# Kernel optimization log

Hardware: AMD Instinct MI355X
Metric: run time of the kernel (lower is better)

Reference implementation:

```python
import jax, jax.numpy as jnp
import numpy as np

GRID_SIZE = 5
SPLINE_ORDER = 3
NB = GRID_SIZE + SPLINE_ORDER          # 8 basis functions
NG = GRID_SIZE + 2 * SPLINE_ORDER + 1  # 12 extended grid points
EPS = 1e-12


def make_grid(in_features):
    h = 2.0 / GRID_SIZE  # grid range [-1, 1]
    pts = (np.arange(-SPLINE_ORDER, GRID_SIZE + SPLINE_ORDER + 1) * h - 1.0).astype(np.float32)
    return jnp.asarray(np.tile(pts[None, :], (in_features, 1)))  # (in, NG)


def bspline_basis(x, grid):
    # x: (B, in), grid: (in, NG) -> (B, in, GRID_SIZE+SPLINE_ORDER)
    xe = x[..., None]
    bases = ((xe >= grid[:, :-1]) & (xe < grid[:, 1:])).astype(x.dtype)
    for k in range(1, SPLINE_ORDER + 1):
        left = (xe - grid[:, :-(k + 1)]) / (grid[:, k:-1] - grid[:, :-(k + 1)]) * bases[..., :-1]
        right = (grid[:, k + 1:] - xe) / (grid[:, k + 1:] - grid[:, 1:-k]) * bases[..., 1:]
        bases = left + right
    return bases


def kan_linear(x, grid, base_w, spline_w):
    # efficient-KAN layer: SiLU base branch + B-spline branch
    base = jax.nn.silu(x) @ base_w.T                      # (B, out)
    basis = bspline_basis(x, grid)                        # (B, in, NB)
    spline = jnp.einsum('big,oig->bo', basis, spline_w)   # (B, out)
    return base + spline


def l2norm(x):
    return x / jnp.maximum(jnp.linalg.norm(x, axis=1, keepdims=True), EPS)


def setup_inputs() -> dict:
    key = jax.random.key(0)
    ks = jax.random.split(key, 12)
    N = 2048
    x = jax.random.normal(ks[0], (N, 1, 529, 16), dtype=jnp.float32)
    xvaw = jax.random.normal(ks[1], (N, 16), dtype=jnp.float32)
    # KAN([529, 40, 60])
    grid1 = make_grid(529)
    base_w1 = jax.random.normal(ks[2], (40, 529), dtype=jnp.float32) * (1.0 / np.sqrt(529))
    spline_w1 = jax.random.normal(ks[3], (40, 529, NB), dtype=jnp.float32) * 0.1
    grid2 = make_grid(40)
    base_w2 = jax.random.normal(ks[4], (60, 40), dtype=jnp.float32) * (1.0 / np.sqrt(40))
    spline_w2 = jax.random.normal(ks[5], (60, 40, NB), dtype=jnp.float32) * 0.1
    # head: Linear(960,512) -> L2Norm -> spline_activation(512) -> Linear(512,16) -> L2Norm
    lin1_w = jax.random.normal(ks[6], (512, 960), dtype=jnp.float32) * (1.0 / np.sqrt(960))
    lin1_b = jnp.zeros((512,), dtype=jnp.float32)
    act_grid = make_grid(512)
    act_base = jnp.ones((512,), dtype=jnp.float32)
    act_coeff = jax.random.normal(ks[7], (512, NB), dtype=jnp.float32) * 0.1
    lin2_w = jax.random.normal(ks[8], (16, 512), dtype=jnp.float32) * (1.0 / np.sqrt(512))
    lin2_b = jnp.zeros((16,), dtype=jnp.float32)
    return {"x": x, "xvaw": xvaw, "grid1": grid1, "base_w1": base_w1, "spline_w1": spline_w1,
            "grid2": grid2, "base_w2": base_w2, "spline_w2": spline_w2,
            "lin1_w": lin1_w, "lin1_b": lin1_b, "act_grid": act_grid, "act_base": act_base,
            "act_coeff": act_coeff, "lin2_w": lin2_w, "lin2_b": lin2_b}


def reference(x, xvaw, grid1, base_w1, spline_w1, grid2, base_w2, spline_w2,
              lin1_w, lin1_b, act_grid, act_base, act_coeff, lin2_w, lin2_b):
    N = x.shape[0]
    W = x.shape[3]  # 16
    xa = jnp.transpose(x[:, 0], (2, 0, 1)).reshape(W * N, 529)  # batched over all W slices
    h = kan_linear(xa, grid1, base_w1, spline_w1)               # (W*N, 40)
    h = kan_linear(h, grid2, base_w2, spline_w2)                # (W*N, 60)
    h = jnp.transpose(h.reshape(W, N, 60), (1, 2, 0)).reshape(N, 60 * W)  # (N, 960)
    h = h @ lin1_w.T + lin1_b
    h = l2norm(h)
    # per-dim spline activation (KAN-style single activation)
    basis = bspline_basis(h, act_grid)                          # (N, 512, NB)
    h = act_base * jax.nn.silu(h) + jnp.einsum('bdg,dg->bd', basis, act_coeff)
    h = h @ lin2_w.T + lin2_b
    return l2norm(h)
```

## Files before the change

kernel.cpp:

```cpp
#include <hip/hip_runtime.h>


typedef short bf16x8 __attribute__((ext_vector_type(8)));
typedef float f32x16 __attribute__((ext_vector_type(16)));

__device__ __forceinline__ float siluf(float x) { return x / (1.f + __expf(-x)); }

__device__ __forceinline__ unsigned short f2bf_rne(float v) {
    union { float f; unsigned u; } a; a.f = v;
    return (unsigned short)((a.u + 0x7fffu + ((a.u >> 16) & 1u)) >> 16);
}
__device__ __forceinline__ float bf2f(unsigned short h) {
    union { unsigned u; float f; } a; a.u = ((unsigned)h) << 16;
    return a.f;
}

__device__ __forceinline__ void bspline8(float x, float fm[8]) {
    float tpos = (x + 2.2f) * 2.5f;
    float fc = floorf(tpos);
    int c = (int)fc;
    float u = tpos - fc;
    bool valid = (c >= 0) && (c <= 10);
    float om = 1.f - u;
    float u2 = u * u, u3 = u2 * u;
    float W0 = om * om * om * (1.f / 6.f);
    float W1 = (3.f * u3 - 6.f * u2 + 4.f) * (1.f / 6.f);
    float W2 = (-3.f * u3 + 3.f * u2 + 3.f * u + 1.f) * (1.f / 6.f);
    float W3 = u3 * (1.f / 6.f);
#pragma unroll
    for (int m = 0; m < 8; ++m) {
        int d = c - m;
        float v = (d == 3) ? W0 : 0.f;
        v = (d == 2) ? W1 : v;
        v = (d == 1) ? W2 : v;
        v = (d == 0) ? W3 : v;
        fm[m] = valid ? v : 0.f;
    }
}

__global__ __launch_bounds__(256) void k_prep(
    const float* __restrict__ base_w1, const float* __restrict__ spline_w1,
    const float* __restrict__ base_w2, const float* __restrict__ spline_w2,
    const float* __restrict__ lin1_w,
    unsigned short* __restrict__ bhi, unsigned short* __restrict__ blo,
    unsigned short* __restrict__ whi, unsigned short* __restrict__ wlo,
    float* __restrict__ w2t) {
    int gid = blockIdx.x * 256 + threadIdx.x;
    int stride = gridDim.x * 256;
    for (int idx = gid; idx < 529 * 2 * 512; idx += stride) {
        int j = idx & 7;
        int l = (idx >> 3) & 63;
        int nti = idx >> 9;
        int nt = nti & 1;
        int i = nti >> 1;
        int q = ((l >> 5) << 3) + j;
        int o = nt * 32 + (l & 31);
        float val = 0.f;
        if (o < 40 && q <= 8)
            val = (q == 0) ? base_w1[o * 529 + i]
                           : spline_w1[(o * 529 + i) * 8 + (q - 1)];
        unsigned short h = f2bf_rne(val);
        bhi[idx] = h;
        blo[idx] = f2bf_rne(val - bf2f(h));
    }
    for (int idx = gid; idx < 60 * 16 * 512; idx += stride) {
        int j = idx & 7;
        int l = (idx >> 3) & 63;
        int ctdq = idx >> 9;
        int ct = ctdq & 15;
        int dq = ctdq >> 4;
        int k = dq * 16 + ((l >> 5) << 3) + j;
        int u = ct * 32 + (l & 31);
        float val = lin1_w[(size_t)u * 960 + k];
        unsigned short h = f2bf_rne(val);
        whi[idx] = h;
        wlo[idx] = f2bf_rne(val - bf2f(h));
    }
    for (int idx = gid; idx < 40 * 540; idx += stride) {
        int i = idx / 540;
        int rem = idx - i * 540;
        int q = rem / 60;
        int o = rem - q * 60;
        w2t[idx] = (q == 0) ? base_w2[o * 40 + i]
                            : spline_w2[(o * 40 + i) * 8 + (q - 1)];
    }
}

__global__ __launch_bounds__(256) void k_l1(
    const float* __restrict__ x, const unsigned short* __restrict__ bhi,
    const unsigned short* __restrict__ blo, _Float16* __restrict__ h1p) {
    int t = threadIdx.x;
    int l = t & 63;
    int wv = t >> 6;
    int rb = blockIdx.x & 255;
    int split = blockIdx.x >> 8;
    int gr0 = rb * 128 + wv * 32;
    int col = l & 31;
    int g2 = l >> 5;
    int gr = gr0 + col;
    const float* xrow = x + (size_t)(gr >> 4) * 8464 + (gr & 15);

    f32x16 acc0, acc1;
#pragma unroll
    for (int r = 0; r < 16; ++r) { acc0[r] = 0.f; acc1[r] = 0.f; }

    int i_lo = split * 89;
    int i_hi = i_lo + 89 < 529 ? i_lo + 89 : 529;

    float xv_nxt = xrow[(size_t)i_lo * 16];
#pragma unroll 1
    for (int i = i_lo; i < i_hi; ++i) {
        float xv = xv_nxt;
        int inx = i + 1;
        xv_nxt = (inx < i_hi) ? xrow[(size_t)inx * 16] : 0.f;

        float s0 = siluf(xv);
        float fm[8];
        bspline8(xv, fm);

        float av[8];
        av[0] = g2 ? fm[7] : s0;
#pragma unroll
        for (int j = 1; j < 8; ++j) av[j] = g2 ? 0.f : fm[j - 1];

        bf16x8 ahi, alo;
#pragma unroll
        for (int j = 0; j < 8; ++j) {
            union { float f; unsigned u; } a; a.f = av[j];
            unsigned short h = (unsigned short)(a.u >> 16);
            ahi[j] = (short)h;
            union { float f; unsigned u; } r; r.f = av[j] - bf2f(h);
            alo[j] = (short)(r.u >> 16);
        }

        const bf16x8* bh = (const bf16x8*)(bhi + ((size_t)i * 2) * 512 + (size_t)l * 8);
        const bf16x8* bl = (const bf16x8*)(blo + ((size_t)i * 2) * 512 + (size_t)l * 8);
        bf16x8 bh0 = bh[0], bh1 = bh[64];
        bf16x8 bl0 = bl[0], bl1 = bl[64];

        acc0 = __builtin_amdgcn_mfma_f32_32x32x16_bf16(ahi, bh0, acc0, 0, 0, 0);
        acc1 = __builtin_amdgcn_mfma_f32_32x32x16_bf16(ahi, bh1, acc1, 0, 0, 0);
        acc0 = __builtin_amdgcn_mfma_f32_32x32x16_bf16(ahi, bl0, acc0, 0, 0, 0);
        acc1 = __builtin_amdgcn_mfma_f32_32x32x16_bf16(ahi, bl1, acc1, 0, 0, 0);
        acc0 = __builtin_amdgcn_mfma_f32_32x32x16_bf16(alo, bh0, acc0, 0, 0, 0);
        acc1 = __builtin_amdgcn_mfma_f32_32x32x16_bf16(alo, bh1, acc1, 0, 0, 0);
    }

    _Float16* hp = h1p + (size_t)split * 1310720;
#pragma unroll
    for (int reg = 0; reg < 16; ++reg) {
        int rl = (reg & 3) + 8 * (reg >> 2) + 4 * g2;
        size_t g = (size_t)(gr0 + rl);
        hp[g * 40 + col] = (_Float16)acc0[reg];
        if (col < 8) hp[g * 40 + 32 + col] = (_Float16)acc1[reg];
    }
}

__global__ __launch_bounds__(256) void k_l2(
    const _Float16* __restrict__ h1p, const float* __restrict__ w2t,
    float* __restrict__ h2d) {
    __shared__ float lds[256 * 41];
    int t = threadIdx.x;
    int rc = blockIdx.x >> 2;
    int oq = blockIdx.x & 3;
    size_t base = (size_t)rc * 10240;

#pragma unroll 1
    for (int e = t; e < 10240; e += 256) {
        int r = e / 40;
        int i = e - r * 40;
        float v = (float)h1p[base + e];
        v += (float)h1p[1310720 + base + e];
        v += (float)h1p[2621440 + base + e];
        v += (float)h1p[3932160 + base + e];
        v += (float)h1p[5242880 + base + e];
        v += (float)h1p[6553600 + base + e];
        lds[r * 41 + i] = v;
    }
    __syncthreads();

    float acc[15];
#pragma unroll
    for (int oo = 0; oo < 15; ++oo) acc[oo] = 0.f;

#pragma unroll 1
    for (int i = 0; i < 40; ++i) {
        float hv = lds[t * 41 + i];
        float f[9];
        f[0] = siluf(hv);
        bspline8(hv, f + 1);
        const float* wp = w2t + i * 540 + oq * 15;
#pragma unroll
        for (int q = 0; q < 9; ++q) {
            float fv = f[q];
#pragma unroll
            for (int oo = 0; oo < 15; ++oo)
                acc[oo] = fmaf(fv, wp[q * 60 + oo], acc[oo]);
        }
    }
    int gr = rc * 256 + t;
    int n = gr >> 4, w = gr & 15;
    float* op = h2d + (size_t)n * 960 + w;
#pragma unroll
    for (int oo = 0; oo < 15; ++oo)
        op[(size_t)(oq * 15 + oo) * 16] = acc[oo];
}

__global__ __launch_bounds__(256) void k3(
    const float* __restrict__ h2d, const unsigned short* __restrict__ whi,
    const unsigned short* __restrict__ wlo, const float* __restrict__ lin1_b,
    float* __restrict__ h3) {
    int t = threadIdx.x;
    int l = t & 63;
    int wv = t >> 6;
    int rt = blockIdx.x >> 2;
    int ct = (blockIdx.x & 3) * 4 + wv;
    int col = l & 31;
    int g2 = l >> 5;
    int row = rt * 32 + col;
    const float* hrow = h2d + (size_t)row * 960 + g2 * 8;

    f32x16 acc;
#pragma unroll
    for (int r = 0; r < 16; ++r) acc[r] = 0.f;

#pragma unroll 1
    for (int dq = 0; dq < 60; ++dq) {
        float4 a0 = *(const float4*)(hrow + dq * 16);
        float4 a1 = *(const float4*)(hrow + dq * 16 + 4);
        float av[8] = {a0.x, a0.y, a0.z, a0.w, a1.x, a1.y, a1.z, a1.w};

        bf16x8 ahi, alo;
#pragma unroll
        for (int j = 0; j < 8; ++j) {
            union { float f; unsigned u; } a; a.f = av[j];
            unsigned short h = (unsigned short)(a.u >> 16);
            ahi[j] = (short)h;
            union { float f; unsigned u; } r; r.f = av[j] - bf2f(h);
            alo[j] = (short)(r.u >> 16);
        }

        size_t boff = ((size_t)(dq * 16 + ct) * 64 + l) * 8;
        bf16x8 bhv = *(const bf16x8*)(whi + boff);
        bf16x8 blv = *(const bf16x8*)(wlo + boff);

        acc = __builtin_amdgcn_mfma_f32_32x32x16_bf16(ahi, bhv, acc, 0, 0, 0);
        acc = __builtin_amdgcn_mfma_f32_32x32x16_bf16(ahi, blv, acc, 0, 0, 0);
        acc = __builtin_amdgcn_mfma_f32_32x32x16_bf16(alo, bhv, acc, 0, 0, 0);
    }

    int u = ct * 32 + col;
    float bu = lin1_b[u];
#pragma unroll
    for (int reg = 0; reg < 16; ++reg) {
        int rl = (reg & 3) + 8 * (reg >> 2) + 4 * g2;
        h3[(size_t)(rt * 32 + rl) * 512 + u] = acc[reg] + bu;
    }
}

__global__ __launch_bounds__(512) void k4(
    const float* __restrict__ h3, const float* __restrict__ act_base,
    const float* __restrict__ act_coeff, const float* __restrict__ lin2_w,
    const float* __restrict__ lin2_b, float* __restrict__ out) {
    int t = threadIdx.x;
    int wv = t >> 6, lane = t & 63;
    int n = blockIdx.x * 8 + wv;
    const float* hr = h3 + (size_t)n * 512;

    float xv[8];
#pragma unroll
    for (int k = 0; k < 8; ++k) xv[k] = hr[lane + 64 * k];
    float ss = 0.f;
#pragma unroll
    for (int k = 0; k < 8; ++k) ss = fmaf(xv[k], xv[k], ss);
#pragma unroll
    for (int d = 1; d < 64; d <<= 1) ss += __shfl_xor(ss, d, 64);
    float scale = 1.f / fmaxf(sqrtf(ss), 1e-12f);

    float act[8];
#pragma unroll
    for (int k = 0; k < 8; ++k) {
        int u = lane + 64 * k;
        float hn = xv[k] * scale;
        float s = siluf(hn);
        float fm[8];
        bspline8(hn, fm);
        float4 c0 = *(const float4*)(act_coeff + (size_t)u * 8);
        float4 c1 = *(const float4*)(act_coeff + (size_t)u * 8 + 4);
        float a = act_base[u] * s;
        a = fmaf(fm[0], c0.x, a);
        a = fmaf(fm[1], c0.y, a);
        a = fmaf(fm[2], c0.z, a);
        a = fmaf(fm[3], c0.w, a);
        a = fmaf(fm[4], c1.x, a);
        a = fmaf(fm[5], c1.y, a);
        a = fmaf(fm[6], c1.z, a);
        a = fmaf(fm[7], c1.w, a);
        act[k] = a;
    }

    float y = 0.f;
#pragma unroll
    for (int v = 0; v < 16; ++v) {
        float pv = 0.f;
#pragma unroll
        for (int k = 0; k < 8; ++k)
            pv = fmaf(act[k], lin2_w[v * 512 + lane + 64 * k], pv);
#pragma unroll
        for (int d = 1; d < 64; d <<= 1) pv += __shfl_xor(pv, d, 64);
        if (lane == v) y = pv + lin2_b[v];
    }
    float qq = y * y;
#pragma unroll
    for (int d = 1; d < 16; d <<= 1) qq += __shfl_xor(qq, d, 64);
    float sc2 = 1.f / fmaxf(sqrtf(qq), 1e-12f);
    if (lane < 16)
        out[(size_t)n * 16 + lane] = y * sc2;
}

extern "C" void kernel_launch(void* const* d_in, const int* in_sizes, int n_in,
                              void* d_out, int out_size, void* d_ws,
                              size_t ws_size, hipStream_t stream) {
    auto find = [&](int sz, int occur) -> const float* {
        int seen = 0;
        for (int i = 0; i < n_in; ++i) {
            if (in_sizes[i] == sz) {
                if (seen == occur) return (const float*)d_in[i];
                ++seen;
            }
        }
        return nullptr;
    };
    const float* x         = find(17334272, 0);
    const float* base_w1   = find(21160, 0);
    const float* spline_w1 = find(169280, 0);
    const float* base_w2   = find(2400, 0);
    const float* spline_w2 = find(19200, 0);
    const float* lin1_w    = find(491520, 0);
    const float* lin1_b    = find(512, 0);
    const float* act_base  = find(512, 1);
    const float* act_coeff = find(4096, 0);
    const float* lin2_w    = find(8192, 0);
    const float* lin2_b    = find(16, 0);
    if (!x || !base_w1 || !spline_w1 || !base_w2 || !spline_w2 || !lin1_w ||
        !lin1_b || !act_base || !act_coeff || !lin2_w || !lin2_b) {
        x         = (const float*)d_in[0];
        base_w1   = (const float*)d_in[3];
        spline_w1 = (const float*)d_in[4];
        base_w2   = (const float*)d_in[6];
        spline_w2 = (const float*)d_in[7];
        lin1_w    = (const float*)d_in[8];
        lin1_b    = (const float*)d_in[9];
        act_base  = (const float*)d_in[11];
        act_coeff = (const float*)d_in[12];
        lin2_w    = (const float*)d_in[13];
        lin2_b    = (const float*)d_in[14];
    }

    char* ws = (char*)d_ws;
    float* w2t = (float*)ws;
    unsigned short* whi = (unsigned short*)(ws + 86400);
    unsigned short* wlo = (unsigned short*)(ws + 1069440);
    float* h2d = (float*)(ws + 2052480);
    unsigned short* bhi = (unsigned short*)(ws + 2052480);
    unsigned short* blo = bhi + 541696;
    _Float16* h1p = (_Float16*)(ws + 9916800);
    float* h3 = (float*)(ws + 25645440);

    k_prep<<<1024, 256, 0, stream>>>(base_w1, spline_w1, base_w2, spline_w2,
                                     lin1_w, bhi, blo, whi, wlo, w2t);
    k_l1<<<1536, 256, 0, stream>>>(x, bhi, blo, h1p);
    k_l2<<<512, 256, 0, stream>>>(h1p, w2t, h2d);
    k3<<<256, 256, 0, stream>>>(h2d, whi, wlo, lin1_b, h3);
    k4<<<256, 512, 0, stream>>>(h3, act_base, act_coeff, lin2_w, lin2_b,
                                (float*)d_out);
}
```

Before: 379.9 us.

## Pack layer-1 K dimension densely: separate base and spline GEMMs over packed inputs

Layer 1 used to spend one 16-wide MFMA K step per input feature with half the slots padded. It now runs a base GEMM over 16 inputs per step (34 steps) and a spline GEMM that packs two inputs' 8 basis values per step (265 steps). The weight prep builds matching repacked bf16 hi/lo tables. This roughly halves the MFMA count and weight loads. k_l2 now reduces the split partials with vectorized per-row f16x8 loads and drops the __syncthreads, and the hi/lo bf16 split packing uses bit masks. The risks are the extra x loads (each x is read twice) and the more complex selection logic for the basis values.

```diff
diff --git a/kernel.cpp b/kernel.cpp
--- a/kernel.cpp
+++ b/kernel.cpp
@@ -2,7 +2,9 @@
 
 
 typedef short bf16x8 __attribute__((ext_vector_type(8)));
+typedef unsigned u32x4 __attribute__((ext_vector_type(4)));
 typedef float f32x16 __attribute__((ext_vector_type(16)));
+typedef _Float16 f16x8 __attribute__((ext_vector_type(8)));
 
 __device__ __forceinline__ float siluf(float x) { return x / (1.f + __expf(-x)); }
 
@@ -42,26 +44,39 @@
     const float* __restrict__ base_w1, const float* __restrict__ spline_w1,
     const float* __restrict__ base_w2, const float* __restrict__ spline_w2,
     const float* __restrict__ lin1_w,
-    unsigned short* __restrict__ bhi, unsigned short* __restrict__ blo,
+    unsigned short* __restrict__ bsh, unsigned short* __restrict__ bsl,
+    unsigned short* __restrict__ bbh, unsigned short* __restrict__ bbl,
     unsigned short* __restrict__ whi, unsigned short* __restrict__ wlo,
     float* __restrict__ w2t) {
     int gid = blockIdx.x * 256 + threadIdx.x;
     int stride = gridDim.x * 256;
-    for (int idx = gid; idx < 529 * 2 * 512; idx += stride) {
+    for (int idx = gid; idx < 265 * 2 * 512; idx += stride) {
         int j = idx & 7;
         int l = (idx >> 3) & 63;
-        int nti = idx >> 9;
-        int nt = nti & 1;
-        int i = nti >> 1;
-        int q = ((l >> 5) << 3) + j;
+        int ntkk = idx >> 9;
+        int nt = ntkk & 1;
+        int kk = ntkk >> 1;
+        int i = 2 * kk + (l >> 5);
         int o = nt * 32 + (l & 31);
         float val = 0.f;
-        if (o < 40 && q <= 8)
-            val = (q == 0) ? base_w1[o * 529 + i]
-                           : spline_w1[(o * 529 + i) * 8 + (q - 1)];
+        if (o < 40 && i < 529) val = spline_w1[(o * 529 + i) * 8 + j];
         unsigned short h = f2bf_rne(val);
-        bhi[idx] = h;
-        blo[idx] = f2bf_rne(val - bf2f(h));
+        bsh[idx] = h;
+        bsl[idx] = f2bf_rne(val - bf2f(h));
+    }
+    for (int idx = gid; idx < 34 * 2 * 512; idx += stride) {
+        int j = idx & 7;
+        int l = (idx >> 3) & 63;
+        int ntkk = idx >> 9;
+        int nt = ntkk & 1;
+        int kk = ntkk >> 1;
+        int i = kk * 16 + ((l >> 5) << 3) + j;
+        int o = nt * 32 + (l & 31);
+        float val = 0.f;
+        if (o < 40 && i < 529) val = base_w1[o * 529 + i];
+        unsigned short h = f2bf_rne(val);
+        bbh[idx] = h;
+        bbl[idx] = f2bf_rne(val - bf2f(h));
     }
     for (int idx = gid; idx < 60 * 16 * 512; idx += stride) {
         int j = idx & 7;
@@ -87,8 +102,10 @@
 }
 
 __global__ __launch_bounds__(256) void k_l1(
-    const float* __restrict__ x, const unsigned short* __restrict__ bhi,
-    const unsigned short* __restrict__ blo, _Float16* __restrict__ h1p) {
+    const float* __restrict__ x,
+    const unsigned short* __restrict__ bsh, const unsigned short* __restrict__ bsl,
+    const unsigned short* __restrict__ bbh, const unsigned short* __restrict__ bbl,
+    _Float16* __restrict__ h1p) {
     int t = threadIdx.x;
     int l = t & 63;
     int wv = t >> 6;
@@ -99,51 +116,113 @@
     int g2 = l >> 5;
     int gr = gr0 + col;
     const float* xrow = x + (size_t)(gr >> 4) * 8464 + (gr & 15);
+    const unsigned M = 0xFFFF0000u;
 
     f32x16 acc0, acc1;
 #pragma unroll
     for (int r = 0; r < 16; ++r) { acc0[r] = 0.f; acc1[r] = 0.f; }
 
-    int i_lo = split * 89;
-    int i_hi = i_lo + 89 < 529 ? i_lo + 89 : 529;
-
-    float xv_nxt = xrow[(size_t)i_lo * 16];
+    int sk0 = split * 6;
+    int sk1 = sk0 + 6; if (sk1 > 34) sk1 = 34;
 #pragma unroll 1
-    for (int i = i_lo; i < i_hi; ++i) {
-        float xv = xv_nxt;
-        int inx = i + 1;
-        xv_nxt = (inx < i_hi) ? xrow[(size_t)inx * 16] : 0.f;
-
-        float s0 = siluf(xv);
-        float fm[8];
-        bspline8(xv, fm);
-
-        float av[8];
-        av[0] = g2 ? fm[7] : s0;
-#pragma unroll
-        for (int j = 1; j < 8; ++j) av[j] = g2 ? 0.f : fm[j - 1];
-
-        bf16x8 ahi, alo;
-#pragma unroll
-        for (int j = 0; j < 8; ++j) {
-            union { float f; unsigned u; } a; a.f = av[j];
-            unsigned short h = (unsigned short)(a.u >> 16);
-            ahi[j] = (short)h;
-            union { float f; unsigned u; } r; r.f = av[j] - bf2f(h);
-            alo[j] = (short)(r.u >> 16);
-        }
-
-        const bf16x8* bh = (const bf16x8*)(bhi + ((size_t)i * 2) * 512 + (size_t)l * 8);
-        const bf16x8* bl = (const bf16x8*)(blo + ((size_t)i * 2) * 512 + (size_t)l * 8);
-        bf16x8 bh0 = bh[0], bh1 = bh[64];
-        bf16x8 bl0 = bl[0], bl1 = bl[64];
-
-        acc0 = __builtin_amdgcn_mfma_f32_32x32x16_bf16(ahi, bh0, acc0, 0, 0, 0);
-        acc1 = __builtin_amdgcn_mfma_f32_32x32x16_bf16(ahi, bh1, acc1, 0, 0, 0);
-        acc0 = __builtin_amdgcn_mfma_f32_32x32x16_bf16(ahi, bl0, acc0, 0, 0, 0);
-        acc1 = __builtin_amdgcn_mfma_f32_32x32x16_bf16(ahi, bl1, acc1, 0, 0, 0);
-        acc0 = __builtin_amdgcn_mfma_f32_32x32x16_bf16(alo, bh0, acc0, 0, 0, 0);
-        acc1 = __builtin_amdgcn_mfma_f32_32x32x16_bf16(alo, bh1, acc1, 0, 0, 0);
+    for (int kk = sk0; kk < sk1; ++kk) {
+        int ib = kk * 16 + 8 * g2;
+        unsigned hw[4], lw[4];
+#pragma unroll
+        for (int p = 0; p < 4; ++p) {
+            int i0 = ib + 2 * p, i1 = i0 + 1;
+            float x0 = (i0 < 529) ? xrow[(size_t)i0 * 16] : 0.f;
+            float x1 = (i1 < 529) ? xrow[(size_t)i1 * 16] : 0.f;
+            float s0 = siluf(x0), s1 = siluf(x1);
+            unsigned u0 = __float_as_uint(s0), u1 = __float_as_uint(s1);
+            hw[p] = (u0 >> 16) | (u1 & M);
+            float r0 = s0 - __uint_as_float(u0 & M);
+            float r1 = s1 - __uint_as_float(u1 & M);
+            lw[p] = (__float_as_uint(r0) >> 16) | (__float_as_uint(r1) & M);
+        }
+        u32x4 hv = {hw[0], hw[1], hw[2], hw[3]};
+        u32x4 lv = {lw[0], lw[1], lw[2], lw[3]};
+        bf16x8 ah = __builtin_bit_cast(bf16x8, hv);
+        bf16x8 al = __builtin_bit_cast(bf16x8, lv);
+
+        size_t boff = ((size_t)kk * 2) * 512 + (size_t)l * 8;
+        bf16x8 bh0 = *(const bf16x8*)(bbh + boff);
+        bf16x8 bh1 = *(const bf16x8*)(bbh + boff + 512);
+        bf16x8 bl0 = *(const bf16x8*)(bbl + boff);
+        bf16x8 bl1 = *(const bf16x8*)(bbl + boff + 512);
+
+        acc0 = __builtin_amdgcn_mfma_f32_32x32x16_bf16(ah, bh0, acc0, 0, 0, 0);
+        acc1 = __builtin_amdgcn_mfma_f32_32x32x16_bf16(ah, bh1, acc1, 0, 0, 0);
+        acc0 = __builtin_amdgcn_mfma_f32_32x32x16_bf16(ah, bl0, acc0, 0, 0, 0);
+        acc1 = __builtin_amdgcn_mfma_f32_32x32x16_bf16(ah, bl1, acc1, 0, 0, 0);
+        acc0 = __builtin_amdgcn_mfma_f32_32x32x16_bf16(al, bh0, acc0, 0, 0, 0);
+        acc1 = __builtin_amdgcn_mfma_f32_32x32x16_bf16(al, bh1, acc1, 0, 0, 0);
+    }
+
+    int pk0 = split * 45;
+    int pk1 = pk0 + 45; if (pk1 > 265) pk1 = 265;
+#pragma unroll 1
+    for (int kk = pk0; kk < pk1; ++kk) {
+        int i0 = 2 * kk + g2;
+        float xv = (i0 < 529) ? xrow[(size_t)i0 * 16] : 0.f;
+        float tpos = (xv + 2.2f) * 2.5f;
+        float fc = floorf(tpos);
+        int c = (int)fc;
+        float u = tpos - fc;
+        bool valid = (c >= 0) && (c <= 10) && (i0 < 529);
+        int cI = valid ? c : 1000;
+        float om = 1.f - u;
+        float u2 = u * u, u3 = u2 * u;
+        float W0 = om * om * om * (1.f / 6.f);
+        float W1 = (3.f * u3 - 6.f * u2 + 4.f) * (1.f / 6.f);
+        float W2 = (-3.f * u3 + 3.f * u2 + 3.f * u + 1.f) * (1.f / 6.f);
+        float W3 = u3 * (1.f / 6.f);
+
+        unsigned ub0 = __float_as_uint(W0), ub1 = __float_as_uint(W1);
+        unsigned ub2 = __float_as_uint(W2), ub3 = __float_as_uint(W3);
+        float L0 = W0 - __uint_as_float(ub0 & M);
+        float L1 = W1 - __uint_as_float(ub1 & M);
+        float L2 = W2 - __uint_as_float(ub2 & M);
+        float L3 = W3 - __uint_as_float(ub3 & M);
+        unsigned ul0 = __float_as_uint(L0), ul1 = __float_as_uint(L1);
+        unsigned ul2 = __float_as_uint(L2), ul3 = __float_as_uint(L3);
+
+        unsigned PH[5], PL[5];
+        PH[0] = ub3 >> 16;              PL[0] = ul3 >> 16;
+        PH[1] = (ub2 >> 16) | (ub3 & M); PL[1] = (ul2 >> 16) | (ul3 & M);
+        PH[2] = (ub1 >> 16) | (ub2 & M); PL[2] = (ul1 >> 16) | (ul2 & M);
+        PH[3] = (ub0 >> 16) | (ub1 & M); PL[3] = (ul0 >> 16) | (ul1 & M);
+        PH[4] = ub0 & M;                PL[4] = ul0 & M;
+
+        unsigned hw[4], lw[4];
+#pragma unroll
+        for (int p = 0; p < 4; ++p) {
+            int s = cI - 2 * p;
+            unsigned h = 0, lo = 0;
+            h = (s == 0) ? PH[0] : h;  lo = (s == 0) ? PL[0] : lo;
+            h = (s == 1) ? PH[1] : h;  lo = (s == 1) ? PL[1] : lo;
+            h = (s == 2) ? PH[2] : h;  lo = (s == 2) ? PL[2] : lo;
+            h = (s == 3) ? PH[3] : h;  lo = (s == 3) ? PL[3] : lo;
+            h = (s == 4) ? PH[4] : h;  lo = (s == 4) ? PL[4] : lo;
+            hw[p] = h; lw[p] = lo;
+        }
+        u32x4 hv = {hw[0], hw[1], hw[2], hw[3]};
+        u32x4 lv = {lw[0], lw[1], lw[2], lw[3]};
+        bf16x8 ah = __builtin_bit_cast(bf16x8, hv);
+        bf16x8 al = __builtin_bit_cast(bf16x8, lv);
+
+        size_t boff = ((size_t)kk * 2) * 512 + (size_t)l * 8;
+        bf16x8 bh0 = *(const bf16x8*)(bsh + boff);
+        bf16x8 bh1 = *(const bf16x8*)(bsh + boff + 512);
+        bf16x8 bl0 = *(const bf16x8*)(bsl + boff);
+        bf16x8 bl1 = *(const bf16x8*)(bsl + boff + 512);
+
+        acc0 = __builtin_amdgcn_mfma_f32_32x32x16_bf16(ah, bh0, acc0, 0, 0, 0);
+        acc1 = __builtin_amdgcn_mfma_f32_32x32x16_bf16(ah, bh1, acc1, 0, 0, 0);
+        acc0 = __builtin_amdgcn_mfma_f32_32x32x16_bf16(ah, bl0, acc0, 0, 0, 0);
+        acc1 = __builtin_amdgcn_mfma_f32_32x32x16_bf16(ah, bl1, acc1, 0, 0, 0);
+        acc0 = __builtin_amdgcn_mfma_f32_32x32x16_bf16(al, bh0, acc0, 0, 0, 0);
+        acc1 = __builtin_amdgcn_mfma_f32_32x32x16_bf16(al, bh1, acc1, 0, 0, 0);
     }
 
     _Float16* hp = h1p + (size_t)split * 1310720;
@@ -163,21 +242,24 @@
     int t = threadIdx.x;
     int rc = blockIdx.x >> 2;
     int oq = blockIdx.x & 3;
-    size_t base = (size_t)rc * 10240;
-
-#pragma unroll 1
-    for (int e = t; e < 10240; e += 256) {
-        int r = e / 40;
-        int i = e - r * 40;
-        float v = (float)h1p[base + e];
-        v += (float)h1p[1310720 + base + e];
-        v += (float)h1p[2621440 + base + e];
-        v += (float)h1p[3932160 + base + e];
-        v += (float)h1p[5242880 + base + e];
-        v += (float)h1p[6553600 + base + e];
-        lds[r * 41 + i] = v;
-    }
-    __syncthreads();
+    int gr = rc * 256 + t;
+
+    const f16x8* p0 = (const f16x8*)(h1p + (size_t)gr * 40);
+#pragma unroll
+    for (int cc = 0; cc < 5; ++cc) {
+        f16x8 v = p0[cc];
+        float s[8];
+#pragma unroll
+        for (int j = 0; j < 8; ++j) s[j] = (float)v[j];
+#pragma unroll
+        for (int sp = 1; sp < 6; ++sp) {
+            f16x8 w = p0[(size_t)sp * 163840 + cc];
+#pragma unroll
+            for (int j = 0; j < 8; ++j) s[j] += (float)w[j];
+        }
+#pragma unroll
+        for (int j = 0; j < 8; ++j) lds[t * 41 + cc * 8 + j] = s[j];
+    }
 
     float acc[15];
 #pragma unroll
@@ -198,7 +280,6 @@
                 acc[oo] = fmaf(fv, wp[q * 60 + oo], acc[oo]);
         }
     }
-    int gr = rc * 256 + t;
     int n = gr >> 4, w = gr & 15;
     float* op = h2d + (size_t)n * 960 + w;
 #pragma unroll
@@ -219,6 +300,7 @@
     int g2 = l >> 5;
     int row = rt * 32 + col;
     const float* hrow = h2d + (size_t)row * 960 + g2 * 8;
+    const unsigned M = 0xFFFF0000u;
 
     f32x16 acc;
 #pragma unroll
@@ -230,15 +312,20 @@
         float4 a1 = *(const float4*)(hrow + dq * 16 + 4);
         float av[8] = {a0.x, a0.y, a0.z, a0.w, a1.x, a1.y, a1.z, a1.w};
 
-        bf16x8 ahi, alo;
-#pragma unroll
-        for (int j = 0; j < 8; ++j) {
-            union { float f; unsigned u; } a; a.f = av[j];
-            unsigned short h = (unsigned short)(a.u >> 16);
-            ahi[j] = (short)h;
-            union { float f; unsigned u; } r; r.f = av[j] - bf2f(h);
-            alo[j] = (short)(r.u >> 16);
-        }
+        unsigned hw[4], lw[4];
+#pragma unroll
+        for (int p = 0; p < 4; ++p) {
+            unsigned u0 = __float_as_uint(av[2 * p]);
+            unsigned u1 = __float_as_uint(av[2 * p + 1]);
+            hw[p] = (u0 >> 16) | (u1 & M);
+            float r0 = av[2 * p] - __uint_as_float(u0 & M);
+            float r1 = av[2 * p + 1] - __uint_as_float(u1 & M);
+            lw[p] = (__float_as_uint(r0) >> 16) | (__float_as_uint(r1) & M);
+        }
+        u32x4 hv = {hw[0], hw[1], hw[2], hw[3]};
+        u32x4 lv = {lw[0], lw[1], lw[2], lw[3]};
+        bf16x8 ahi = __builtin_bit_cast(bf16x8, hv);
+        bf16x8 alo = __builtin_bit_cast(bf16x8, lv);
 
         size_t boff = ((size_t)(dq * 16 + ct) * 64 + l) * 8;
         bf16x8 bhv = *(const bf16x8*)(whi + boff);
@@ -362,14 +449,16 @@
     unsigned short* whi = (unsigned short*)(ws + 86400);
     unsigned short* wlo = (unsigned short*)(ws + 1069440);
     float* h2d = (float*)(ws + 2052480);
-    unsigned short* bhi = (unsigned short*)(ws + 2052480);
-    unsigned short* blo = bhi + 541696;
+    unsigned short* bsh = (unsigned short*)(ws + 2052480);
+    unsigned short* bsl = (unsigned short*)(ws + 2595200);
+    unsigned short* bbh = (unsigned short*)(ws + 3137920);
+    unsigned short* bbl = (unsigned short*)(ws + 3207552);
     _Float16* h1p = (_Float16*)(ws + 9916800);
     float* h3 = (float*)(ws + 25645440);
 
     k_prep<<<1024, 256, 0, stream>>>(base_w1, spline_w1, base_w2, spline_w2,
-                                     lin1_w, bhi, blo, whi, wlo, w2t);
-    k_l1<<<1536, 256, 0, stream>>>(x, bhi, blo, h1p);
+                                     lin1_w, bsh, bsl, bbh, bbl, whi, wlo, w2t);
+    k_l1<<<1536, 256, 0, stream>>>(x, bsh, bsl, bbh, bbl, h1p);
     k_l2<<<512, 256, 0, stream>>>(h1p, w2t, h2d);
     k3<<<256, 256, 0, stream>>>(h2d, whi, wlo, lin1_b, h3);
     k4<<<256, 512, 0, stream>>>(h3, act_base, act_coeff, lin2_w, lin2_b,
```

After: 328.4 us. 1.16x faster.
